# Kernel optimization log

Hardware: AMD Instinct MI355X
Metric: run time of the kernel (lower is better)

Reference implementation:

```python
import jax, jax.numpy as jnp
import numpy as np

EPS = 1e-6

def elu_feature_map(x):
    return jax.nn.elu(x) + 1.0

def setup_inputs() -> dict:
    key = jax.random.key(0)
    kq, kk, kv = jax.random.split(key, 3)
    B, N, L, S, H, D, M = 4, 8, 1024, 1024, 8, 64, 64
    queries = jax.random.normal(kq, (B, N, L, H, D), dtype=jnp.float32)
    keys = jax.random.normal(kk, (B, N, S, H, D), dtype=jnp.float32)
    values = jax.random.normal(kv, (B, N, S, H, M), dtype=jnp.float32)
    key_mask = jnp.ones((B, S), dtype=jnp.float32)  # key_lengths.float_matrix (all valid)
    return {"queries": queries, "keys": keys, "values": values, "key_mask": key_mask}

def reference(queries, keys, values, key_mask):
    # Q: [B,N,L,H,D], K: [B,N,S,H,D], V: [B,N,S,H,M], key_mask: [B,S]
    Q = elu_feature_map(queries)
    K = elu_feature_map(keys) * key_mask[:, None, :, None, None]
    # KV state: [B,N,H,M,D]
    KV = jnp.einsum('bnshd,bnshm->bnhmd', K, values)
    # normalizer: [B,N,L,H]
    Z = 1.0 / (jnp.einsum('bnlhd,bnhd->bnlh', Q, K.sum(axis=2)) + EPS)
    # output: [B,N,L,H,M]
    V = jnp.einsum('bnlhd,bnhmd,bnlh->bnlhm', Q, KV, Z)
    return V
```

## Files before the change

kernel.cpp:

```cpp
#include <hip/hip_runtime.h>
#include <hip/hip_bf16.h>


constexpr int Bc = 4, Nc = 8, Hc = 8;
constexpr int Lc = 1024, Sc = 1024, Dc = 64, Mc = 64;
constexpr int HD = Hc * Dc;
constexpr int GROUPS = Bc * Nc * Hc;
constexpr int LSPLITS = 4;
constexpr int LROWS = Lc / LSPLITS;
constexpr int PARTIAL = Dc * Mc + Dc;
constexpr int NTL = LROWS / 64;
constexpr int PADD = 68;
constexpr float EPSF = 1e-6f;

typedef __attribute__((ext_vector_type(8))) __bf16 bf16x8;
typedef __attribute__((ext_vector_type(4))) float f32x4;

__device__ __forceinline__ float elup1(float x) {
    return x > 0.0f ? x + 1.0f : __expf(x);
}
__device__ __forceinline__ unsigned short f2bf(float f) {
    unsigned u = __builtin_bit_cast(unsigned, f);
    u += 0x7fffu + ((u >> 16) & 1u);
    return (unsigned short)(u >> 16);
}
__device__ __forceinline__ float bf2f(unsigned short h) {
    return __builtin_bit_cast(float, (unsigned)h << 16);
}
__device__ __forceinline__ void splitbf(float x, unsigned short& h, unsigned short& l) {
    h = f2bf(x);
    l = f2bf(x - bf2f(h));
}
__device__ __forceinline__ unsigned pack2(unsigned short lo, unsigned short hi) {
    return (unsigned)lo | ((unsigned)hi << 16);
}
__device__ __forceinline__ bf16x8 ones_frag() {
    union { bf16x8 v; unsigned short s[8]; } u;
    #pragma unroll
    for (int i = 0; i < 8; ++i) u.s[i] = 0x3F80;
    return u.v;
}

template<int NSPL>
__global__ void __launch_bounds__(256, 4)
la_kv_direct(const float* __restrict__ Kg, const float* __restrict__ Vg,
             const float* __restrict__ Mg, float* __restrict__ ws)
{
    constexpr int SR = Sc / NSPL;
    constexpr int NT = SR / 32;

    const int t    = threadIdx.x;
    const int lane = t & 63;
    const int w    = t >> 6;
    const int frow = lane & 15;
    const int kg   = lane >> 4;
    const int g    = blockIdx.y;
    const int sp   = blockIdx.x;
    const int h    = g & 7;
    const int bn   = g >> 3;
    const int b    = g >> 6;

    const size_t rowbase = (size_t)bn * Sc * HD + (size_t)h * Dc;
    const size_t mbase   = (size_t)b * Sc;
    const int    sbase   = sp * SR;

    f32x4 acc[4], aks;
    #pragma unroll
    for (int ms = 0; ms < 4; ++ms) acc[ms] = (f32x4){0.f, 0.f, 0.f, 0.f};
    aks = (f32x4){0.f, 0.f, 0.f, 0.f};
    const bf16x8 ones = ones_frag();

    union uf { bf16x8 v; unsigned short s[8]; };

    #pragma unroll 1
    for (int it = 0; it < NT; ++it) {
        const int sb = sbase + it * 32 + 8 * kg;
        const float* kp = Kg + rowbase + (size_t)sb * HD + 16 * w + frow;
        const float* vp = Vg + rowbase + (size_t)sb * HD + frow;
        const float* mp = Mg + mbase + sb;

        float ka[8], mk[8], vb[4][8];
        #pragma unroll
        for (int j = 0; j < 8; ++j) {
            ka[j] = kp[j * HD];
            mk[j] = mp[j];
        }
        #pragma unroll
        for (int ms = 0; ms < 4; ++ms)
            #pragma unroll
            for (int j = 0; j < 8; ++j)
                vb[ms][j] = vp[j * HD + 16 * ms];

        uf kh, kl;
        #pragma unroll
        for (int j = 0; j < 8; ++j) {
            const float a = elup1(ka[j]) * mk[j];
            splitbf(a, kh.s[j], kl.s[j]);
        }
        aks = __builtin_amdgcn_mfma_f32_16x16x32_bf16(kh.v, ones, aks, 0, 0, 0);
        aks = __builtin_amdgcn_mfma_f32_16x16x32_bf16(kl.v, ones, aks, 0, 0, 0);
        #pragma unroll
        for (int ms = 0; ms < 4; ++ms) {
            uf vh, vl;
            #pragma unroll
            for (int j = 0; j < 8; ++j)
                splitbf(vb[ms][j], vh.s[j], vl.s[j]);
            acc[ms] = __builtin_amdgcn_mfma_f32_16x16x32_bf16(kh.v, vh.v, acc[ms], 0, 0, 0);
            acc[ms] = __builtin_amdgcn_mfma_f32_16x16x32_bf16(kh.v, vl.v, acc[ms], 0, 0, 0);
            acc[ms] = __builtin_amdgcn_mfma_f32_16x16x32_bf16(kl.v, vh.v, acc[ms], 0, 0, 0);
        }
    }

    float* outp = ws + (size_t)(g * NSPL + sp) * PARTIAL;
    #pragma unroll
    for (int ms = 0; ms < 4; ++ms)
        #pragma unroll
        for (int r = 0; r < 4; ++r)
            outp[(16 * w + 4 * (lane >> 4) + r) * Mc + 16 * ms + frow] = acc[ms][r];

    if (frow == 0) {
        #pragma unroll
        for (int r = 0; r < 4; ++r)
            outp[Dc * Mc + 16 * w + 4 * (lane >> 4) + r] = aks[r];
    }
}

template<int NSPL>
__global__ void __launch_bounds__(256, 4)
la_out_mfma(const float* __restrict__ Qg, const float* __restrict__ ws,
            float* __restrict__ Og)
{
    __shared__ unsigned short kvh[Mc][PADD];
    __shared__ unsigned short kvl[Mc][PADD];
    __shared__ unsigned short ksh[64];
    __shared__ unsigned short ksl[64];
    __shared__ unsigned short qhh[64][PADD];
    __shared__ unsigned short qll[64][PADD];

    const int t    = threadIdx.x;
    const int tx   = t & 15;
    const int tyq  = t >> 4;
    const int lane = t & 63;
    const int w    = t >> 6;
    const int g    = blockIdx.y;
    const int ls   = blockIdx.x;
    const int h    = g & 7;
    const int bn   = g >> 3;

    const size_t rowbase = (size_t)bn * Lc * HD + (size_t)h * Dc;
    const float* pw = ws + (size_t)g * NSPL * PARTIAL;
    const int lbase = ls * LROWS;

    float4 qr[4];
    auto loadB = [&](int it) {
        const int l0 = lbase + it * 64 + 4 * tyq;
        #pragma unroll
        for (int j = 0; j < 4; ++j)
            qr[j] = *reinterpret_cast<const float4*>(Qg + rowbase + (size_t)(l0 + j) * HD + 4 * tx);
    };
    auto storeB = [&]() {
        #pragma unroll
        for (int j = 0; j < 4; ++j) {
            const int r = 4 * tyq + j;
            const float q[4] = {qr[j].x, qr[j].y, qr[j].z, qr[j].w};
            unsigned short h0, l0, h1, l1, h2, l2, h3, l3;
            splitbf(elup1(q[0]), h0, l0);
            splitbf(elup1(q[1]), h1, l1);
            splitbf(elup1(q[2]), h2, l2);
            splitbf(elup1(q[3]), h3, l3);
            uint2 ph, pl;
            ph.x = pack2(h0, h1); ph.y = pack2(h2, h3);
            pl.x = pack2(l0, l1); pl.y = pack2(l2, l3);
            *reinterpret_cast<uint2*>(&qhh[r][4 * tx]) = ph;
            *reinterpret_cast<uint2*>(&qll[r][4 * tx]) = pl;
        }
    };

    loadB(0);
    #pragma unroll
    for (int e = 0; e < 16; ++e) {
        const int idx = t + 256 * e;
        float s = 0.f;
        #pragma unroll
        for (int sp = 0; sp < NSPL; ++sp) s += pw[sp * PARTIAL + idx];
        unsigned short hh, ll;
        splitbf(s, hh, ll);
        kvh[idx & 63][idx >> 6] = hh;
        kvl[idx & 63][idx >> 6] = ll;
    }
    if (t < 64) {
        float s = 0.f;
        #pragma unroll
        for (int sp = 0; sp < NSPL; ++sp) s += pw[sp * PARTIAL + Dc * Mc + t];
        unsigned short hh, ll;
        splitbf(s, hh, ll);
        ksh[t] = hh;
        ksl[t] = ll;
    }
    storeB();
    __syncthreads();

    const int fcol = 8 * (lane >> 4);
    const int frow = lane & 15;
    const size_t obase = (size_t)bn * Lc * HD + (size_t)h * Mc;

    for (int it = 0; it < NTL; ++it) {
        if (it + 1 < NTL) loadB(it + 1);
        union { bf16x8 v; uint2 u[2]; } fah0, fal0, fah1, fal1;
        {
            const uint2* p;
            p = reinterpret_cast<const uint2*>(&qhh[16 * w + frow][fcol]);      fah0.u[0] = p[0]; fah0.u[1] = p[1];
            p = reinterpret_cast<const uint2*>(&qll[16 * w + frow][fcol]);      fal0.u[0] = p[0]; fal0.u[1] = p[1];
            p = reinterpret_cast<const uint2*>(&qhh[16 * w + frow][32 + fcol]); fah1.u[0] = p[0]; fah1.u[1] = p[1];
            p = reinterpret_cast<const uint2*>(&qll[16 * w + frow][32 + fcol]); fal1.u[0] = p[0]; fal1.u[1] = p[1];
        }
        f32x4 acc[4], accz;
        #pragma unroll
        for (int ms = 0; ms < 4; ++ms) acc[ms] = (f32x4){0.f, 0.f, 0.f, 0.f};
        accz = (f32x4){0.f, 0.f, 0.f, 0.f};

        #pragma unroll
        for (int ks = 0; ks < 2; ++ks) {
            const bf16x8 fh = ks ? fah1.v : fah0.v;
            const bf16x8 fl = ks ? fal1.v : fal0.v;
            #pragma unroll
            for (int ms = 0; ms < 4; ++ms) {
                union { bf16x8 v; uint2 u[2]; } fbh, fbl;
                const uint2* ph = reinterpret_cast<const uint2*>(&kvh[16 * ms + frow][32 * ks + fcol]);
                fbh.u[0] = ph[0]; fbh.u[1] = ph[1];
                const uint2* pl = reinterpret_cast<const uint2*>(&kvl[16 * ms + frow][32 * ks + fcol]);
                fbl.u[0] = pl[0]; fbl.u[1] = pl[1];
                acc[ms] = __builtin_amdgcn_mfma_f32_16x16x32_bf16(fh, fbh.v, acc[ms], 0, 0, 0);
                acc[ms] = __builtin_amdgcn_mfma_f32_16x16x32_bf16(fh, fbl.v, acc[ms], 0, 0, 0);
                acc[ms] = __builtin_amdgcn_mfma_f32_16x16x32_bf16(fl, fbh.v, acc[ms], 0, 0, 0);
            }
            union { bf16x8 v; uint2 u[2]; } fzh, fzl;
            const uint2* ph = reinterpret_cast<const uint2*>(&ksh[32 * ks + fcol]);
            fzh.u[0] = ph[0]; fzh.u[1] = ph[1];
            const uint2* pl = reinterpret_cast<const uint2*>(&ksl[32 * ks + fcol]);
            fzl.u[0] = pl[0]; fzl.u[1] = pl[1];
            accz = __builtin_amdgcn_mfma_f32_16x16x32_bf16(fh, fzh.v, accz, 0, 0, 0);
            accz = __builtin_amdgcn_mfma_f32_16x16x32_bf16(fh, fzl.v, accz, 0, 0, 0);
            accz = __builtin_amdgcn_mfma_f32_16x16x32_bf16(fl, fzh.v, accz, 0, 0, 0);
        }

        const int lt = lbase + it * 64 + 16 * w + 4 * (lane >> 4);
        #pragma unroll
        for (int r = 0; r < 4; ++r) {
            const float z = 1.0f / (accz[r] + EPSF);
            const size_t ro = obase + (size_t)(lt + r) * HD + frow;
            #pragma unroll
            for (int ms = 0; ms < 4; ++ms)
                Og[ro + 16 * ms] = acc[ms][r] * z;
        }
        __syncthreads();
        if (it + 1 < NTL) storeB();
        __syncthreads();
    }
}

__global__ void __launch_bounds__(256, 1)
la_fused_kernel(const float* __restrict__ Qg, const float* __restrict__ Kg,
                const float* __restrict__ Vg, const float* __restrict__ Mg,
                float* __restrict__ Og)
{
    __shared__ float lk[32][Dc];
    __shared__ float lv[32][Mc];
    __shared__ float kvt[Dc][Mc];
    __shared__ float ksm[Dc];
    __shared__ float qt[Dc][64];

    const int t  = threadIdx.x;
    const int tx = t & 15;
    const int ty = t >> 4;
    const int g  = blockIdx.x;
    const int h  = g & 7;
    const int bn = g >> 3;
    const int b  = g >> 6;

    const size_t rowbase = (size_t)bn * Sc * HD + (size_t)h * Dc;
    const size_t mbase   = (size_t)b * Sc;

    const int d0 = tx * 4, m0 = ty * 4, c4 = tx * 4, r0 = ty;

    float acc[4][4] = {{0.f,0.f,0.f,0.f},{0.f,0.f,0.f,0.f},{0.f,0.f,0.f,0.f},{0.f,0.f,0.f,0.f}};
    float ks[4] = {0.f, 0.f, 0.f, 0.f};
    float4 kr[2], vr[2];
    float  mr[2];

    auto loadA = [&](int it) {
        const int s0 = it * 32;
        #pragma unroll
        for (int k = 0; k < 2; ++k) {
            const int r = r0 + 16 * k;
            const size_t off = rowbase + (size_t)(s0 + r) * HD + c4;
            kr[k] = *reinterpret_cast<const float4*>(Kg + off);
            vr[k] = *reinterpret_cast<const float4*>(Vg + off);
            mr[k] = Mg[mbase + s0 + r];
        }
    };
    auto storeA = [&]() {
        #pragma unroll
        for (int k = 0; k < 2; ++k) {
            const int r = r0 + 16 * k;
            float4 kk;
            kk.x = elup1(kr[k].x) * mr[k];
            kk.y = elup1(kr[k].y) * mr[k];
            kk.z = elup1(kr[k].z) * mr[k];
            kk.w = elup1(kr[k].w) * mr[k];
            *reinterpret_cast<float4*>(&lk[r][c4]) = kk;
            *reinterpret_cast<float4*>(&lv[r][c4]) = vr[k];
        }
    };

    loadA(0);
    storeA();
    __syncthreads();
    for (int it = 0; it < Sc / 32; ++it) {
        if (it + 1 < Sc / 32) loadA(it + 1);
        #pragma unroll 8
        for (int r = 0; r < 32; ++r) {
            const float4 k4 = *reinterpret_cast<const float4*>(&lk[r][d0]);
            const float4 v4 = *reinterpret_cast<const float4*>(&lv[r][m0]);
            const float kk[4] = {k4.x, k4.y, k4.z, k4.w};
            const float vv[4] = {v4.x, v4.y, v4.z, v4.w};
            ks[0] += kk[0]; ks[1] += kk[1]; ks[2] += kk[2]; ks[3] += kk[3];
            #pragma unroll
            for (int i = 0; i < 4; ++i)
                #pragma unroll
                for (int j = 0; j < 4; ++j)
                    acc[i][j] += kk[i] * vv[j];
        }
        __syncthreads();
        if (it + 1 < Sc / 32) storeA();
        __syncthreads();
    }

    #pragma unroll
    for (int i = 0; i < 4; ++i) {
        float4 w;
        w.x = acc[i][0]; w.y = acc[i][1]; w.z = acc[i][2]; w.w = acc[i][3];
        *reinterpret_cast<float4*>(&kvt[d0 + i][m0]) = w;
    }
    if (ty == 0) {
        #pragma unroll
        for (int i = 0; i < 4; ++i) ksm[d0 + i] = ks[i];
    }
    __syncthreads();

    float4 qr[4];
    auto loadB = [&](int it) {
        const int l0 = it * 64;
        #pragma unroll
        for (int k = 0; k < 4; ++k) {
            const int r = r0 + 16 * k;
            const size_t off = rowbase + (size_t)(l0 + r) * HD + c4;
            qr[k] = *reinterpret_cast<const float4*>(Qg + off);
        }
    };
    const int swzw = (tx & 7) << 2;
    auto storeB = [&]() {
        #pragma unroll
        for (int k = 0; k < 4; ++k) {
            const int r = r0 + 16 * k;
            const int lidx = r ^ swzw;
            qt[c4 + 0][lidx] = elup1(qr[k].x);
            qt[c4 + 1][lidx] = elup1(qr[k].y);
            qt[c4 + 2][lidx] = elup1(qr[k].z);
            qt[c4 + 3][lidx] = elup1(qr[k].w);
        }
    };

    loadB(0);
    storeB();
    __syncthreads();
    for (int it = 0; it < Lc / 64; ++it) {
        if (it + 1 < Lc / 64) loadB(it + 1);
        float accB[4][4] = {{0.f,0.f,0.f,0.f},{0.f,0.f,0.f,0.f},{0.f,0.f,0.f,0.f},{0.f,0.f,0.f,0.f}};
        float za[4] = {0.f, 0.f, 0.f, 0.f};
        #pragma unroll 8
        for (int d = 0; d < Dc; ++d) {
            const int swz = ((d >> 2) & 7) << 2;
            const float4 q4  = *reinterpret_cast<const float4*>(&qt[d][(4 * ty) ^ swz]);
            const float4 kv4 = *reinterpret_cast<const float4*>(&kvt[d][4 * tx]);
            const float kd = ksm[d];
            const float qq[4] = {q4.x, q4.y, q4.z, q4.w};
            const float kv[4] = {kv4.x, kv4.y, kv4.z, kv4.w};
            #pragma unroll
            for (int i = 0; i < 4; ++i) {
                za[i] += qq[i] * kd;
                #pragma unroll
                for (int j = 0; j < 4; ++j)
                    accB[i][j] += qq[i] * kv[j];
            }
        }
        const int l0 = it * 64;
        const size_t obase = (size_t)bn * Lc * HD + (size_t)h * Mc;
        #pragma unroll
        for (int i = 0; i < 4; ++i) {
            const int l = l0 + 4 * ty + i;
            const float z = 1.0f / (za[i] + EPSF);
            float4 o;
            o.x = accB[i][0] * z; o.y = accB[i][1] * z;
            o.z = accB[i][2] * z; o.w = accB[i][3] * z;
            *reinterpret_cast<float4*>(Og + obase + (size_t)l * HD + 4 * tx) = o;
        }
        __syncthreads();
        if (it + 1 < Lc / 64) storeB();
        __syncthreads();
    }
}

extern "C" void kernel_launch(void* const* d_in, const int* in_sizes, int n_in,
                              void* d_out, int out_size, void* d_ws, size_t ws_size,
                              hipStream_t stream) {
    const float* Qg = (const float*)d_in[0];
    const float* Kg = (const float*)d_in[1];
    const float* Vg = (const float*)d_in[2];
    const float* Mg = (const float*)d_in[3];
    float* Og = (float*)d_out;

    const size_t need4 = (size_t)GROUPS * 4 * PARTIAL * sizeof(float);
    if (ws_size >= need4) {
        float* ws = (float*)d_ws;
        hipLaunchKernelGGL((la_kv_direct<4>), dim3(4, GROUPS), dim3(256), 0, stream,
                           Kg, Vg, Mg, ws);
        hipLaunchKernelGGL((la_out_mfma<4>), dim3(LSPLITS, GROUPS), dim3(256), 0, stream,
                           Qg, ws, Og);
    } else {
        hipLaunchKernelGGL(la_fused_kernel, dim3(GROUPS), dim3(256), 0, stream,
                           Qg, Kg, Vg, Mg, Og);
    }
}
```

Measured before the change: 80.89 us.

## Stage K/V through LDS with coalesced float4 loads and double S-splits

Replaces the KV-state kernel's strided scalar global loads with coalesced float4 loads of K and V. These are converted to split bf16 hi/lo pairs and stored transposed into padded shared memory, and MFMA fragments are then read from LDS. The S dimension is split 8 ways instead of 4 when the workspace allows, and launch bounds now target 8 blocks per SU, to raise parallelism. The cost is two barriers per iteration, extra LDS traffic, and more partials for the output kernel to reduce.

```diff
diff --git a/kernel.cpp b/kernel.cpp
--- a/kernel.cpp
+++ b/kernel.cpp
@@ -10,6 +10,7 @@
 constexpr int LROWS = Lc / LSPLITS;
 constexpr int PARTIAL = Dc * Mc + Dc;
 constexpr int NTL = LROWS / 64;
+constexpr int PADS = 36;
 constexpr int PADD = 68;
 constexpr float EPSF = 1e-6f;
 
@@ -42,18 +43,23 @@
 }
 
 template<int NSPL>
-__global__ void __launch_bounds__(256, 4)
-la_kv_direct(const float* __restrict__ Kg, const float* __restrict__ Vg,
-             const float* __restrict__ Mg, float* __restrict__ ws)
+__global__ void __launch_bounds__(256, 8)
+la_kv_mfma(const float* __restrict__ Kg, const float* __restrict__ Vg,
+           const float* __restrict__ Mg, float* __restrict__ ws)
 {
     constexpr int SR = Sc / NSPL;
     constexpr int NT = SR / 32;
 
+    __shared__ unsigned short kth[Dc][PADS];
+    __shared__ unsigned short ktl[Dc][PADS];
+    __shared__ unsigned short vth[Dc][PADS];
+    __shared__ unsigned short vtl[Dc][PADS];
+
     const int t    = threadIdx.x;
+    const int tx   = t & 15;
+    const int tyq  = t >> 4;
     const int lane = t & 63;
     const int w    = t >> 6;
-    const int frow = lane & 15;
-    const int kg   = lane >> 4;
     const int g    = blockIdx.y;
     const int sp   = blockIdx.x;
     const int h    = g & 7;
@@ -70,45 +76,63 @@
     aks = (f32x4){0.f, 0.f, 0.f, 0.f};
     const bf16x8 ones = ones_frag();
 
-    union uf { bf16x8 v; unsigned short s[8]; };
-
-    #pragma unroll 1
+    const int fcol = 8 * (lane >> 4);
+    const int frow = lane & 15;
+
     for (int it = 0; it < NT; ++it) {
-        const int sb = sbase + it * 32 + 8 * kg;
-        const float* kp = Kg + rowbase + (size_t)sb * HD + 16 * w + frow;
-        const float* vp = Vg + rowbase + (size_t)sb * HD + frow;
-        const float* mp = Mg + mbase + sb;
-
-        float ka[8], mk[8], vb[4][8];
-        #pragma unroll
-        for (int j = 0; j < 8; ++j) {
-            ka[j] = kp[j * HD];
-            mk[j] = mp[j];
-        }
-        #pragma unroll
-        for (int ms = 0; ms < 4; ++ms)
-            #pragma unroll
-            for (int j = 0; j < 8; ++j)
-                vb[ms][j] = vp[j * HD + 16 * ms];
-
-        uf kh, kl;
-        #pragma unroll
-        for (int j = 0; j < 8; ++j) {
-            const float a = elup1(ka[j]) * mk[j];
-            splitbf(a, kh.s[j], kl.s[j]);
-        }
-        aks = __builtin_amdgcn_mfma_f32_16x16x32_bf16(kh.v, ones, aks, 0, 0, 0);
-        aks = __builtin_amdgcn_mfma_f32_16x16x32_bf16(kl.v, ones, aks, 0, 0, 0);
-        #pragma unroll
-        for (int ms = 0; ms < 4; ++ms) {
-            uf vh, vl;
-            #pragma unroll
-            for (int j = 0; j < 8; ++j)
-                splitbf(vb[ms][j], vh.s[j], vl.s[j]);
-            acc[ms] = __builtin_amdgcn_mfma_f32_16x16x32_bf16(kh.v, vh.v, acc[ms], 0, 0, 0);
-            acc[ms] = __builtin_amdgcn_mfma_f32_16x16x32_bf16(kh.v, vl.v, acc[ms], 0, 0, 0);
-            acc[ms] = __builtin_amdgcn_mfma_f32_16x16x32_bf16(kl.v, vh.v, acc[ms], 0, 0, 0);
-        }
+        const int s0 = sbase + it * 32 + 2 * tyq;
+        const size_t off = rowbase + (size_t)s0 * HD + 4 * tx;
+        const float4 k0 = *reinterpret_cast<const float4*>(Kg + off);
+        const float4 k1 = *reinterpret_cast<const float4*>(Kg + off + HD);
+        const float4 v0 = *reinterpret_cast<const float4*>(Vg + off);
+        const float4 v1 = *reinterpret_cast<const float4*>(Vg + off + HD);
+        const float2 m2 = *reinterpret_cast<const float2*>(Mg + mbase + s0);
+
+        {
+            const float ka0[4] = {k0.x, k0.y, k0.z, k0.w};
+            const float ka1[4] = {k1.x, k1.y, k1.z, k1.w};
+            const float va0[4] = {v0.x, v0.y, v0.z, v0.w};
+            const float va1[4] = {v1.x, v1.y, v1.z, v1.w};
+            #pragma unroll
+            for (int i = 0; i < 4; ++i) {
+                const float a0 = elup1(ka0[i]) * m2.x;
+                const float a1 = elup1(ka1[i]) * m2.y;
+                unsigned short h0, l0, h1, l1;
+                splitbf(a0, h0, l0);
+                splitbf(a1, h1, l1);
+                *reinterpret_cast<unsigned*>(&kth[4 * tx + i][2 * tyq]) = pack2(h0, h1);
+                *reinterpret_cast<unsigned*>(&ktl[4 * tx + i][2 * tyq]) = pack2(l0, l1);
+                unsigned short vh0, vl0, vh1, vl1;
+                splitbf(va0[i], vh0, vl0);
+                splitbf(va1[i], vh1, vl1);
+                *reinterpret_cast<unsigned*>(&vth[4 * tx + i][2 * tyq]) = pack2(vh0, vh1);
+                *reinterpret_cast<unsigned*>(&vtl[4 * tx + i][2 * tyq]) = pack2(vl0, vl1);
+            }
+        }
+        __syncthreads();
+
+        {
+            union { bf16x8 v; uint2 u[2]; } fah, fal;
+            const uint2* ph = reinterpret_cast<const uint2*>(&kth[16 * w + frow][fcol]);
+            fah.u[0] = ph[0]; fah.u[1] = ph[1];
+            const uint2* pl = reinterpret_cast<const uint2*>(&ktl[16 * w + frow][fcol]);
+            fal.u[0] = pl[0]; fal.u[1] = pl[1];
+
+            aks = __builtin_amdgcn_mfma_f32_16x16x32_bf16(fah.v, ones, aks, 0, 0, 0);
+            aks = __builtin_amdgcn_mfma_f32_16x16x32_bf16(fal.v, ones, aks, 0, 0, 0);
+            #pragma unroll
+            for (int ms = 0; ms < 4; ++ms) {
+                union { bf16x8 v; uint2 u[2]; } fbh, fbl;
+                const uint2* qh = reinterpret_cast<const uint2*>(&vth[16 * ms + frow][fcol]);
+                fbh.u[0] = qh[0]; fbh.u[1] = qh[1];
+                const uint2* ql = reinterpret_cast<const uint2*>(&vtl[16 * ms + frow][fcol]);
+                fbl.u[0] = ql[0]; fbl.u[1] = ql[1];
+                acc[ms] = __builtin_amdgcn_mfma_f32_16x16x32_bf16(fah.v, fbh.v, acc[ms], 0, 0, 0);
+                acc[ms] = __builtin_amdgcn_mfma_f32_16x16x32_bf16(fah.v, fbl.v, acc[ms], 0, 0, 0);
+                acc[ms] = __builtin_amdgcn_mfma_f32_16x16x32_bf16(fal.v, fbh.v, acc[ms], 0, 0, 0);
+            }
+        }
+        __syncthreads();
     }
 
     float* outp = ws + (size_t)(g * NSPL + sp) * PARTIAL;
@@ -420,10 +444,17 @@
     const float* Mg = (const float*)d_in[3];
     float* Og = (float*)d_out;
 
+    const size_t need8 = (size_t)GROUPS * 8 * PARTIAL * sizeof(float);
     const size_t need4 = (size_t)GROUPS * 4 * PARTIAL * sizeof(float);
-    if (ws_size >= need4) {
+    if (ws_size >= need8) {
         float* ws = (float*)d_ws;
-        hipLaunchKernelGGL((la_kv_direct<4>), dim3(4, GROUPS), dim3(256), 0, stream,
+        hipLaunchKernelGGL((la_kv_mfma<8>), dim3(8, GROUPS), dim3(256), 0, stream,
+                           Kg, Vg, Mg, ws);
+        hipLaunchKernelGGL((la_out_mfma<8>), dim3(LSPLITS, GROUPS), dim3(256), 0, stream,
+                           Qg, ws, Og);
+    } else if (ws_size >= need4) {
+        float* ws = (float*)d_ws;
+        hipLaunchKernelGGL((la_kv_mfma<4>), dim3(4, GROUPS), dim3(256), 0, stream,
                            Kg, Vg, Mg, ws);
         hipLaunchKernelGGL((la_out_mfma<4>), dim3(LSPLITS, GROUPS), dim3(256), 0, stream,
                            Qg, ws, Og);
```

Measured after the change: 84.02 us. 3.9% more time.

## Stage K/V tiles through LDS with triple-buffered global_load_lds pipeline

Applied to the files above, without the earlier changes.

Rewrites the KV-state kernel so that K and V tiles are loaded into shared memory through direct global-to-LDS DMA loads, with three buffers in flight. Waits use explicit vmcnt counters and barriers. The mask slice is cached in LDS once per block. The aim is to hide global load latency behind the MFMA work and to replace strided per-lane global reads with coalesced 16-byte loads. In exchange it adds about 48KB of LDS per block, which may limit occupancy, and it relies on hand-written waitcnt accounting.

```diff
diff --git a/kernel.cpp b/kernel.cpp
--- a/kernel.cpp
+++ b/kernel.cpp
@@ -16,6 +16,9 @@
 typedef __attribute__((ext_vector_type(8))) __bf16 bf16x8;
 typedef __attribute__((ext_vector_type(4))) float f32x4;
 
+#define AS1C const __attribute__((address_space(1))) void*
+#define AS3  __attribute__((address_space(3))) void*
+
 __device__ __forceinline__ float elup1(float x) {
     return x > 0.0f ? x + 1.0f : __expf(x);
 }
@@ -43,11 +46,15 @@
 
 template<int NSPL>
 __global__ void __launch_bounds__(256, 4)
-la_kv_direct(const float* __restrict__ Kg, const float* __restrict__ Vg,
-             const float* __restrict__ Mg, float* __restrict__ ws)
+la_kv_dma(const float* __restrict__ Kg, const float* __restrict__ Vg,
+          const float* __restrict__ Mg, float* __restrict__ ws)
 {
     constexpr int SR = Sc / NSPL;
     constexpr int NT = SR / 32;
+
+    __shared__ float kf[3][32][64];
+    __shared__ float vf[3][32][64];
+    __shared__ float mlds[SR];
 
     const int t    = threadIdx.x;
     const int lane = t & 63;
@@ -61,8 +68,25 @@
     const int b    = g >> 6;
 
     const size_t rowbase = (size_t)bn * Sc * HD + (size_t)h * Dc;
-    const size_t mbase   = (size_t)b * Sc;
     const int    sbase   = sp * SR;
+
+    if (t < SR) mlds[t] = Mg[(size_t)b * Sc + sbase + t];
+    __syncthreads();
+
+    const int drow = lane >> 4;
+    const int dcol = (lane & 15) * 4;
+
+    auto issue = [&](int it, int buf) {
+        const int s0 = sbase + it * 32 + 8 * w;
+        #pragma unroll
+        for (int q = 0; q < 2; ++q) {
+            const int r = 4 * q;
+            const float* gk = Kg + rowbase + (size_t)(s0 + r + drow) * HD + dcol;
+            const float* gv = Vg + rowbase + (size_t)(s0 + r + drow) * HD + dcol;
+            __builtin_amdgcn_global_load_lds((AS1C)gk, (AS3)&kf[buf][8 * w + r][0], 16, 0, 0);
+            __builtin_amdgcn_global_load_lds((AS1C)gv, (AS3)&vf[buf][8 * w + r][0], 16, 0, 0);
+        }
+    };
 
     f32x4 acc[4], aks;
     #pragma unroll
@@ -72,43 +96,50 @@
 
     union uf { bf16x8 v; unsigned short s[8]; };
 
-    #pragma unroll 1
-    for (int it = 0; it < NT; ++it) {
-        const int sb = sbase + it * 32 + 8 * kg;
-        const float* kp = Kg + rowbase + (size_t)sb * HD + 16 * w + frow;
-        const float* vp = Vg + rowbase + (size_t)sb * HD + frow;
-        const float* mp = Mg + mbase + sb;
-
-        float ka[8], mk[8], vb[4][8];
+    auto compute = [&](int it, int buf) {
+        float ka[8], ml[8];
         #pragma unroll
         for (int j = 0; j < 8; ++j) {
-            ka[j] = kp[j * HD];
-            mk[j] = mp[j];
-        }
-        #pragma unroll
-        for (int ms = 0; ms < 4; ++ms)
-            #pragma unroll
-            for (int j = 0; j < 8; ++j)
-                vb[ms][j] = vp[j * HD + 16 * ms];
-
+            ka[j] = kf[buf][8 * kg + j][16 * w + frow];
+            ml[j] = mlds[it * 32 + 8 * kg + j];
+        }
         uf kh, kl;
         #pragma unroll
-        for (int j = 0; j < 8; ++j) {
-            const float a = elup1(ka[j]) * mk[j];
-            splitbf(a, kh.s[j], kl.s[j]);
-        }
+        for (int j = 0; j < 8; ++j)
+            splitbf(elup1(ka[j]) * ml[j], kh.s[j], kl.s[j]);
         aks = __builtin_amdgcn_mfma_f32_16x16x32_bf16(kh.v, ones, aks, 0, 0, 0);
         aks = __builtin_amdgcn_mfma_f32_16x16x32_bf16(kl.v, ones, aks, 0, 0, 0);
         #pragma unroll
         for (int ms = 0; ms < 4; ++ms) {
+            float vb[8];
+            #pragma unroll
+            for (int j = 0; j < 8; ++j)
+                vb[j] = vf[buf][8 * kg + j][16 * ms + frow];
             uf vh, vl;
             #pragma unroll
             for (int j = 0; j < 8; ++j)
-                splitbf(vb[ms][j], vh.s[j], vl.s[j]);
+                splitbf(vb[j], vh.s[j], vl.s[j]);
             acc[ms] = __builtin_amdgcn_mfma_f32_16x16x32_bf16(kh.v, vh.v, acc[ms], 0, 0, 0);
             acc[ms] = __builtin_amdgcn_mfma_f32_16x16x32_bf16(kh.v, vl.v, acc[ms], 0, 0, 0);
             acc[ms] = __builtin_amdgcn_mfma_f32_16x16x32_bf16(kl.v, vh.v, acc[ms], 0, 0, 0);
         }
+    };
+
+    issue(0, 0);
+    if (NT > 1) issue(1, 1);
+    if (NT > 2) issue(2, 2);
+
+    for (int it = 0; it < NT; ++it) {
+        const int buf = it % 3;
+        const int rem = NT - 1 - it;
+        if (rem >= 2)      asm volatile("s_waitcnt vmcnt(8)" ::: "memory");
+        else if (rem == 1) asm volatile("s_waitcnt vmcnt(4)" ::: "memory");
+        else               asm volatile("s_waitcnt vmcnt(0)" ::: "memory");
+        __builtin_amdgcn_sched_barrier(0);
+        __builtin_amdgcn_s_barrier();
+        compute(it, buf);
+        __builtin_amdgcn_s_barrier();
+        if (it + 3 < NT) issue(it + 3, buf);
     }
 
     float* outp = ws + (size_t)(g * NSPL + sp) * PARTIAL;
@@ -116,12 +147,12 @@
     for (int ms = 0; ms < 4; ++ms)
         #pragma unroll
         for (int r = 0; r < 4; ++r)
-            outp[(16 * w + 4 * (lane >> 4) + r) * Mc + 16 * ms + frow] = acc[ms][r];
+            outp[(16 * w + 4 * kg + r) * Mc + 16 * ms + frow] = acc[ms][r];
 
     if (frow == 0) {
         #pragma unroll
         for (int r = 0; r < 4; ++r)
-            outp[Dc * Mc + 16 * w + 4 * (lane >> 4) + r] = aks[r];
+            outp[Dc * Mc + 16 * w + 4 * kg + r] = aks[r];
     }
 }
 
@@ -423,7 +454,7 @@
     const size_t need4 = (size_t)GROUPS * 4 * PARTIAL * sizeof(float);
     if (ws_size >= need4) {
         float* ws = (float*)d_ws;
-        hipLaunchKernelGGL((la_kv_direct<4>), dim3(4, GROUPS), dim3(256), 0, stream,
+        hipLaunchKernelGGL((la_kv_dma<4>), dim3(4, GROUPS), dim3(256), 0, stream,
                            Kg, Vg, Mg, ws);
         hipLaunchKernelGGL((la_out_mfma<4>), dim3(LSPLITS, GROUPS), dim3(256), 0, stream,
                            Qg, ws, Og);
```

After: 79.58 us. About the same (-1.6%).

## Compute KV state per (b,n) with one wave per head and finer S splits

Applied to the files above, without the earlier changes.

The KV-state kernel now assigns one 512-thread block per (b,n) and S-slice, with each of 8 waves handling one full head (all 64 D columns), instead of one block per head with waves splitting D. Each wave converts its V fragments to bf16 once and reuses them across four D chunks, so V is no longer reloaded and resplit by four waves. The mask load is shared across chunks. More S splits (16 or 8, depending on workspace) are chosen to keep enough blocks in flight. The cost is four times the accumulator registers per wave and more partial results for the output kernel to reduce.

```diff
diff --git a/kernel.cpp b/kernel.cpp
--- a/kernel.cpp
+++ b/kernel.cpp
@@ -6,6 +6,7 @@
 constexpr int Lc = 1024, Sc = 1024, Dc = 64, Mc = 64;
 constexpr int HD = Hc * Dc;
 constexpr int GROUPS = Bc * Nc * Hc;
+constexpr int BN = Bc * Nc;
 constexpr int LSPLITS = 4;
 constexpr int LROWS = Lc / LSPLITS;
 constexpr int PARTIAL = Dc * Mc + Dc;
@@ -42,9 +43,9 @@
 }
 
 template<int NSPL>
-__global__ void __launch_bounds__(256, 4)
-la_kv_direct(const float* __restrict__ Kg, const float* __restrict__ Vg,
-             const float* __restrict__ Mg, float* __restrict__ ws)
+__global__ void __launch_bounds__(512, 2)
+la_kv_fullrow(const float* __restrict__ Kg, const float* __restrict__ Vg,
+              const float* __restrict__ Mg, float* __restrict__ ws)
 {
     constexpr int SR = Sc / NSPL;
     constexpr int NT = SR / 32;
@@ -54,74 +55,80 @@
     const int w    = t >> 6;
     const int frow = lane & 15;
     const int kg   = lane >> 4;
-    const int g    = blockIdx.y;
+    const int bn   = blockIdx.y;
     const int sp   = blockIdx.x;
-    const int h    = g & 7;
-    const int bn   = g >> 3;
-    const int b    = g >> 6;
-
-    const size_t rowbase = (size_t)bn * Sc * HD + (size_t)h * Dc;
-    const size_t mbase   = (size_t)b * Sc;
-    const int    sbase   = sp * SR;
-
-    f32x4 acc[4], aks;
+    const int b    = bn >> 3;
+
+    const size_t hdbase = (size_t)bn * Sc * HD + (size_t)w * Dc;
+    const size_t mbase  = (size_t)b * Sc;
+    const int    sbase  = sp * SR;
+
+    f32x4 acc[4][4];
+    f32x4 aks[4];
     #pragma unroll
-    for (int ms = 0; ms < 4; ++ms) acc[ms] = (f32x4){0.f, 0.f, 0.f, 0.f};
-    aks = (f32x4){0.f, 0.f, 0.f, 0.f};
+    for (int dc = 0; dc < 4; ++dc) {
+        aks[dc] = (f32x4){0.f, 0.f, 0.f, 0.f};
+        #pragma unroll
+        for (int ms = 0; ms < 4; ++ms) acc[dc][ms] = (f32x4){0.f, 0.f, 0.f, 0.f};
+    }
     const bf16x8 ones = ones_frag();
-
     union uf { bf16x8 v; unsigned short s[8]; };
 
     #pragma unroll 1
     for (int it = 0; it < NT; ++it) {
         const int sb = sbase + it * 32 + 8 * kg;
-        const float* kp = Kg + rowbase + (size_t)sb * HD + 16 * w + frow;
-        const float* vp = Vg + rowbase + (size_t)sb * HD + frow;
+        const float* kp = Kg + hdbase + (size_t)sb * HD + frow;
+        const float* vp = Vg + hdbase + (size_t)sb * HD + frow;
         const float* mp = Mg + mbase + sb;
 
-        float ka[8], mk[8], vb[4][8];
-        #pragma unroll
-        for (int j = 0; j < 8; ++j) {
-            ka[j] = kp[j * HD];
-            mk[j] = mp[j];
-        }
+        float ml[8];
+        #pragma unroll
+        for (int j = 0; j < 8; ++j) ml[j] = mp[j];
+
+        uf kh[4], kl[4];
+        #pragma unroll
+        for (int dc = 0; dc < 4; ++dc) {
+            float ka[8];
+            #pragma unroll
+            for (int j = 0; j < 8; ++j) ka[j] = kp[(size_t)j * HD + 16 * dc];
+            #pragma unroll
+            for (int j = 0; j < 8; ++j)
+                splitbf(elup1(ka[j]) * ml[j], kh[dc].s[j], kl[dc].s[j]);
+            aks[dc] = __builtin_amdgcn_mfma_f32_16x16x32_bf16(kh[dc].v, ones, aks[dc], 0, 0, 0);
+            aks[dc] = __builtin_amdgcn_mfma_f32_16x16x32_bf16(kl[dc].v, ones, aks[dc], 0, 0, 0);
+        }
+        #pragma unroll
+        for (int ms = 0; ms < 4; ++ms) {
+            float vb[8];
+            #pragma unroll
+            for (int j = 0; j < 8; ++j) vb[j] = vp[(size_t)j * HD + 16 * ms];
+            uf vh, vl;
+            #pragma unroll
+            for (int j = 0; j < 8; ++j) splitbf(vb[j], vh.s[j], vl.s[j]);
+            #pragma unroll
+            for (int dc = 0; dc < 4; ++dc) {
+                acc[dc][ms] = __builtin_amdgcn_mfma_f32_16x16x32_bf16(kh[dc].v, vh.v, acc[dc][ms], 0, 0, 0);
+                acc[dc][ms] = __builtin_amdgcn_mfma_f32_16x16x32_bf16(kh[dc].v, vl.v, acc[dc][ms], 0, 0, 0);
+                acc[dc][ms] = __builtin_amdgcn_mfma_f32_16x16x32_bf16(kl[dc].v, vh.v, acc[dc][ms], 0, 0, 0);
+            }
+        }
+    }
+
+    float* outp = ws + (size_t)((bn * 8 + w) * NSPL + sp) * PARTIAL;
+    #pragma unroll
+    for (int dc = 0; dc < 4; ++dc)
         #pragma unroll
         for (int ms = 0; ms < 4; ++ms)
             #pragma unroll
-            for (int j = 0; j < 8; ++j)
-                vb[ms][j] = vp[j * HD + 16 * ms];
-
-        uf kh, kl;
-        #pragma unroll
-        for (int j = 0; j < 8; ++j) {
-            const float a = elup1(ka[j]) * mk[j];
-            splitbf(a, kh.s[j], kl.s[j]);
-        }
-        aks = __builtin_amdgcn_mfma_f32_16x16x32_bf16(kh.v, ones, aks, 0, 0, 0);
-        aks = __builtin_amdgcn_mfma_f32_16x16x32_bf16(kl.v, ones, aks, 0, 0, 0);
-        #pragma unroll
-        for (int ms = 0; ms < 4; ++ms) {
-            uf vh, vl;
-            #pragma unroll
-            for (int j = 0; j < 8; ++j)
-                splitbf(vb[ms][j], vh.s[j], vl.s[j]);
-            acc[ms] = __builtin_amdgcn_mfma_f32_16x16x32_bf16(kh.v, vh.v, acc[ms], 0, 0, 0);
-            acc[ms] = __builtin_amdgcn_mfma_f32_16x16x32_bf16(kh.v, vl.v, acc[ms], 0, 0, 0);
-            acc[ms] = __builtin_amdgcn_mfma_f32_16x16x32_bf16(kl.v, vh.v, acc[ms], 0, 0, 0);
-        }
-    }
-
-    float* outp = ws + (size_t)(g * NSPL + sp) * PARTIAL;
-    #pragma unroll
-    for (int ms = 0; ms < 4; ++ms)
-        #pragma unroll
-        for (int r = 0; r < 4; ++r)
-            outp[(16 * w + 4 * (lane >> 4) + r) * Mc + 16 * ms + frow] = acc[ms][r];
+            for (int r = 0; r < 4; ++r)
+                outp[(16 * dc + 4 * kg + r) * Mc + 16 * ms + frow] = acc[dc][ms][r];
 
     if (frow == 0) {
         #pragma unroll
-        for (int r = 0; r < 4; ++r)
-            outp[Dc * Mc + 16 * w + 4 * (lane >> 4) + r] = aks[r];
+        for (int dc = 0; dc < 4; ++dc)
+            #pragma unroll
+            for (int r = 0; r < 4; ++r)
+                outp[Dc * Mc + 16 * dc + 4 * kg + r] = aks[dc][r];
     }
 }
 
@@ -420,10 +427,22 @@
     const float* Mg = (const float*)d_in[3];
     float* Og = (float*)d_out;
 
-    const size_t need4 = (size_t)GROUPS * 4 * PARTIAL * sizeof(float);
-    if (ws_size >= need4) {
-        float* ws = (float*)d_ws;
-        hipLaunchKernelGGL((la_kv_direct<4>), dim3(4, GROUPS), dim3(256), 0, stream,
+    const size_t need16 = (size_t)GROUPS * 16 * PARTIAL * sizeof(float);
+    const size_t need8  = (size_t)GROUPS * 8  * PARTIAL * sizeof(float);
+    const size_t need4  = (size_t)GROUPS * 4  * PARTIAL * sizeof(float);
+    float* ws = (float*)d_ws;
+    if (ws_size >= need16) {
+        hipLaunchKernelGGL((la_kv_fullrow<16>), dim3(16, BN), dim3(512), 0, stream,
+                           Kg, Vg, Mg, ws);
+        hipLaunchKernelGGL((la_out_mfma<16>), dim3(LSPLITS, GROUPS), dim3(256), 0, stream,
+                           Qg, ws, Og);
+    } else if (ws_size >= need8) {
+        hipLaunchKernelGGL((la_kv_fullrow<8>), dim3(8, BN), dim3(512), 0, stream,
+                           Kg, Vg, Mg, ws);
+        hipLaunchKernelGGL((la_out_mfma<8>), dim3(LSPLITS, GROUPS), dim3(256), 0, stream,
+                           Qg, ws, Og);
+    } else if (ws_size >= need4) {
+        hipLaunchKernelGGL((la_kv_fullrow<4>), dim3(4, BN), dim3(512), 0, stream,
                            Kg, Vg, Mg, ws);
         hipLaunchKernelGGL((la_out_mfma<4>), dim3(LSPLITS, GROUPS), dim3(256), 0, stream,
                            Qg, ws, Og);
```

New measurement: 117.0 us. +44.6%, slower.
